# Performance work log

Measured on AMD Instinct MI355X. Metric: run time of the kernel, lower is better.

Reference implementation:

```python
import jax, jax.numpy as jnp
import numpy as np

N_QUBITS = 12
N_LAYERS = 6
BATCH = 1024


def setup_inputs() -> dict:
    key = jax.random.key(0)
    k1, k2, k3, k4 = jax.random.split(key, 4)
    x = jax.random.normal(k1, (BATCH, N_QUBITS), dtype=jnp.float32)
    weights = jax.random.normal(k2, (N_LAYERS, N_QUBITS, 3), dtype=jnp.float32)
    head_w = jax.random.normal(k3, (2, 1), dtype=jnp.float32)
    head_b = jax.random.normal(k4, (2,), dtype=jnp.float32)
    return {"x": x, "weights": weights, "head_w": head_w, "head_b": head_b}


def _apply_1q(state, U, q):
    # state: (B, 2**n) complex64; U: (2,2) or (B,2,2)
    B = state.shape[0]
    st = state.reshape(B, 1 << q, 2, -1)  # isolate qubit q
    if U.ndim == 2:
        new = jnp.einsum('ij,bajc->baic', U, st)
    else:
        new = jnp.einsum('bij,bajc->baic', U, st)
    return new.reshape(B, -1)


def _cnot_adj(state, q):
    # CNOT with control q, target q+1 (adjacent)
    B = state.shape[0]
    st = state.reshape(B, 1 << q, 2, 2, -1)
    new = jnp.concatenate([st[:, :, :1], st[:, :, 1:, ::-1]], axis=2)
    return new.reshape(B, -1)


def _rot_mat(phi, theta, omega):
    # PennyLane Rot = RZ(omega) RY(theta) RZ(phi)
    c = jnp.cos(0.5 * theta)
    s = jnp.sin(0.5 * theta)
    ep = jnp.exp(-0.5j * (phi + omega))
    em = jnp.exp(-0.5j * (phi - omega))
    row0 = jnp.stack([ep * c, -jnp.conj(em) * s])
    row1 = jnp.stack([em * s, jnp.conj(ep) * c])
    return jnp.stack([row0, row1]).astype(jnp.complex64)


def _layer(state, wl, n):
    # wl: (n, 3) Rot params for this layer, then CNOT cascade
    for q in range(n):
        state = _apply_1q(state, _rot_mat(wl[q, 0], wl[q, 1], wl[q, 2]), q)
    for q in range(n - 1):
        state = _cnot_adj(state, q)
    return state


def _circuit(x, weights):
    B, n = x.shape
    state = jnp.zeros((B, 1 << n), jnp.complex64).at[:, 0].set(1.0 + 0.0j)
    # AngleEmbedding: RX(x_q) on qubit q (batched gates)
    for q in range(n):
        h = 0.5 * x[:, q]
        c, s = jnp.cos(h), jnp.sin(h)
        U = jnp.stack([jnp.stack([c, -1j * s], -1),
                       jnp.stack([-1j * s, c], -1)], -2).astype(jnp.complex64)
        state = _apply_1q(state, U, q)
    state = jax.lax.scan(lambda s, wl: (_layer(s, wl, n), None), state, weights)[0]
    # <Z_0>
    p = jnp.abs(state.reshape(B, 2, -1)) ** 2
    return (p[:, 0].sum(-1) - p[:, 1].sum(-1)).astype(jnp.float32)


def reference(x, weights, head_w, head_b):
    z = _circuit(x, weights)            # (B,) expectation values
    q_out = z[:, None]                  # (B, 1)
    return q_out @ head_w.T + head_b    # Linear(1, 2) -> (B, 2)
```

## Files before the change

kernel.cpp:

```cpp
#include <hip/hip_runtime.h>

#define NQ 12
#define NSTATE (1 << NQ)
#define NL 6
#define TPB 512


typedef float f4 __attribute__((ext_vector_type(4)));

struct A2 { float ar, ai, br, bi; };

__device__ __forceinline__ float RL(float v, int idx) {
    return __int_as_float(__builtin_amdgcn_readlane(__float_as_int(v), idx));
}

__device__ __forceinline__ void bf2(A2& s0, A2& s1,
                                    float A, float B, float C, float D) {
    float n0r, n0i, n1r, n1i;
    n0r = fmaf(A, s0.ar, fmaf( B, s0.ai, fmaf(-C, s1.ar,  D * s1.ai)));
    n0i = fmaf(A, s0.ai, fmaf(-B, s0.ar, fmaf(-C, s1.ai, -D * s1.ar)));
    n1r = fmaf(C, s0.ar, fmaf( D, s0.ai, fmaf( A, s1.ar, -B * s1.ai)));
    n1i = fmaf(C, s0.ai, fmaf(-D, s0.ar, fmaf( A, s1.ai,  B * s1.ar)));
    s0.ar = n0r; s0.ai = n0i; s1.ar = n1r; s1.ai = n1i;
    n0r = fmaf(A, s0.br, fmaf( B, s0.bi, fmaf(-C, s1.br,  D * s1.bi)));
    n0i = fmaf(A, s0.bi, fmaf(-B, s0.br, fmaf(-C, s1.bi, -D * s1.br)));
    n1r = fmaf(C, s0.br, fmaf( D, s0.bi, fmaf( A, s1.br, -B * s1.bi)));
    n1i = fmaf(C, s0.bi, fmaf(-D, s0.br, fmaf( A, s1.bi,  B * s1.br)));
    s0.br = n0r; s0.bi = n0i; s1.br = n1r; s1.bi = n1i;
}

#define BF(i,j) bf2(a##i, a##j, A, B, C, D)
#define PK0 BF(0,1); BF(2,3); BF(4,5); BF(6,7);
#define PK1 BF(0,2); BF(1,3); BF(4,6); BF(5,7);
#define PK2 BF(0,4); BF(1,5); BF(2,6); BF(3,7);
#define GATE(qq, P) { const int gi = gb + (qq); \
    const float A = RL(gA, gi), B = RL(gB, gi), \
                C = RL(gC, gi), D = RL(gD, gi); P }

#define LDS4(off) (*(f4*)((char*)st + (off)))
#define LD1(r, ADR) { f4 v = LDS4(ADR(r)); \
    a##r.ar = v.x; a##r.ai = v.y; a##r.br = v.z; a##r.bi = v.w; }
#define ST1(r, ADR) { f4 v = {a##r.ar, a##r.ai, a##r.br, a##r.bi}; \
    LDS4(ADR(r)) = v; }
#define LD8(ADR) { LD1(0,ADR) LD1(1,ADR) LD1(2,ADR) LD1(3,ADR) \
                   LD1(4,ADR) LD1(5,ADR) LD1(6,ADR) LD1(7,ADR) }
#define ST8(ADR) { ST1(0,ADR) ST1(1,ADR) ST1(2,ADR) ST1(3,ADR) \
                   ST1(4,ADR) ST1(5,ADR) ST1(6,ADR) ST1(7,ADR) }

#define ADRA(r)  (ptAb + ((r) << 13))
#define ADRB(r)  (ptBb ^ (((r) << 10) ^ (((r) & 3) << 6)))
#define ADRC(r)  (ptCb ^ (((r) << 7) ^ (((r) >> 1) << 4)))
#define ADRD(r)  (ptDb ^ ((r) << 4))
#define GINV3(r) ((r) ^ ((r) >> 1) ^ ((r) >> 2))
#define ADRDS(r) (ptDSb ^ (GINV3(r) << 4))

#define CM(n, xr, xi, yr, yi) \
    const float n##r = fmaf(xr, yr, -(xi) * (yi)); \
    const float n##i = fmaf(xr, yi,  (xi) * (yr));
#define GCONST(q) const float A##q = RL(gA, q), B##q = RL(gB, q), \
                              C##q = RL(gC, q), D##q = RL(gD, q);
#define VQDEF(q) \
    const float v##q##0r = fmaf(A##q, c##q, -(D##q) * s##q); \
    const float v##q##0i = fmaf(-(B##q), c##q,  (C##q) * s##q); \
    const float v##q##1r = fmaf(C##q, c##q,  (B##q) * s##q); \
    const float v##q##1i = fmaf(-(D##q), c##q, -(A##q) * s##q);
#define WSEL(q, b) \
    const float w##q##r = (tj & (1 << (b))) ? v##q##1r : v##q##0r; \
    const float w##q##i = (tj & (1 << (b))) ? v##q##1i : v##q##0i;
#define SETAMP(g, rp, mm, RE, IM) \
    a##g.RE = fmaf(mm##r, Q##rp##r, -(mm##i) * Q##rp##i); \
    a##g.IM = fmaf(mm##r, Q##rp##i,  (mm##i) * Q##rp##r);

__global__ __launch_bounds__(TPB) void qsim_kernel(
    const float* __restrict__ x,
    const float* __restrict__ w,
    const float* __restrict__ hw,
    const float* __restrict__ hb,
    float* __restrict__ out)
{
    __shared__ f4 st[NSTATE];

    const int t    = threadIdx.x;
    const int lane = t & 63;
    const int e0   = blockIdx.x * 2;

    float gA, gB, gC, gD;
    {
        const float* wl = w + lane * 3;
        float phi = wl[0], th = wl[1], om = wl[2];
        float c, s, ca, sa, cb, sb;
        __sincosf(0.5f * th, &s, &c);
        __sincosf(0.5f * (phi + om), &sa, &ca);
        __sincosf(0.5f * (phi - om), &sb, &cb);
        gA = c * ca; gB = c * sa; gC = s * cb; gD = s * sb;
    }

    const int ptAb = (t ^ ((t >> 4) & 0xF)) << 4;
    const int ptBb = (((((t & 0x1C0) << 3) | (t & 0x3F)) ^ ((t >> 4) & 0x3))) << 4;
    const int ptCb = (((((t & 0x1F8) << 3) | (t & 0x7)) ^ (((t >> 3) & 0x3) << 2))) << 4;
    const int ptDb = ((t << 3) ^ ((t >> 1) & 0xF)) << 4;
    int gv = t << 3;
    gv ^= gv >> 1; gv ^= gv >> 2; gv ^= gv >> 4; gv ^= gv >> 8; gv &= 0xFFF;
    const int ptDSb = (gv ^ ((gv >> 4) & 0xF)) << 4;

    A2 a0, a1, a2, a3, a4, a5, a6, a7;

    #pragma unroll 1
    for (int k = 0; k < 4; ++k) {
        const int gb = (k + 1) * 12;

        if (k == 0) {
            const int tj = t ^ (t >> 1);
            const int t8 = (t >> 8) & 1;
            GCONST(0)  GCONST(1)  GCONST(2)  GCONST(3)
            GCONST(4)  GCONST(5)  GCONST(6)  GCONST(7)
            GCONST(8)  GCONST(9)  GCONST(10) GCONST(11)
            {
                const float* xe = x + e0 * NQ;
                float c0,s0,c1,s1,c2,s2,c3,s3,c4,s4,c5,s5;
                float c6,s6,c7,s7,c8,s8,c9,s9,c10,s10,c11,s11;
                #define EMB(q) __sincosf(0.5f * xe[q], &s##q, &c##q);
                EMB(0) EMB(1) EMB(2) EMB(3) EMB(4)  EMB(5)
                EMB(6) EMB(7) EMB(8) EMB(9) EMB(10) EMB(11)
                VQDEF(4)  WSEL(4,7)  VQDEF(5)  WSEL(5,6)
                VQDEF(6)  WSEL(6,5)  VQDEF(7)  WSEL(7,4)
                VQDEF(8)  WSEL(8,3)  VQDEF(9)  WSEL(9,2)
                VQDEF(10) WSEL(10,1) VQDEF(11) WSEL(11,0)
                CM(m45, w4r, w4i, w5r, w5i)   CM(m67, w6r, w6i, w7r, w7i)
                CM(m89, w8r, w8i, w9r, w9i)   CM(mAB, w10r, w10i, w11r, w11i)
                CM(mP, m45r, m45i, m67r, m67i) CM(mQ, m89r, m89i, mABr, mABi)
                CM(mL, mPr, mPi, mQr, mQi)
                VQDEF(3)
                const float w3ar = t8 ? v31r : v30r, w3ai = t8 ? v31i : v30i;
                const float w3br = t8 ? v30r : v31r, w3bi = t8 ? v30i : v31i;
                CM(q3a, mLr, mLi, w3ar, w3ai)  CM(q3b, mLr, mLi, w3br, w3bi)
                VQDEF(0) VQDEF(1) VQDEF(2)
                CM(H0, v00r, v00i, v10r, v10i) CM(H1, v00r, v00i, v11r, v11i)
                CM(H2, v01r, v01i, v10r, v10i) CM(H3, v01r, v01i, v11r, v11i)
                CM(Q0, H0r, H0i, v20r, v20i)   CM(Q1, H0r, H0i, v21r, v21i)
                CM(Q2, H1r, H1i, v20r, v20i)   CM(Q3, H1r, H1i, v21r, v21i)
                CM(Q4, H2r, H2i, v20r, v20i)   CM(Q5, H2r, H2i, v21r, v21i)
                CM(Q6, H3r, H3i, v20r, v20i)   CM(Q7, H3r, H3i, v21r, v21i)
                SETAMP(0,0,q3a,ar,ai) SETAMP(1,1,q3b,ar,ai)
                SETAMP(2,3,q3a,ar,ai) SETAMP(3,2,q3b,ar,ai)
                SETAMP(4,6,q3a,ar,ai) SETAMP(5,7,q3b,ar,ai)
                SETAMP(6,5,q3a,ar,ai) SETAMP(7,4,q3b,ar,ai)
            }
            {
                const float* xe = x + (e0 + 1) * NQ;
                float c0,s0,c1,s1,c2,s2,c3,s3,c4,s4,c5,s5;
                float c6,s6,c7,s7,c8,s8,c9,s9,c10,s10,c11,s11;
                EMB(0) EMB(1) EMB(2) EMB(3) EMB(4)  EMB(5)
                EMB(6) EMB(7) EMB(8) EMB(9) EMB(10) EMB(11)
                #undef EMB
                VQDEF(4)  WSEL(4,7)  VQDEF(5)  WSEL(5,6)
                VQDEF(6)  WSEL(6,5)  VQDEF(7)  WSEL(7,4)
                VQDEF(8)  WSEL(8,3)  VQDEF(9)  WSEL(9,2)
                VQDEF(10) WSEL(10,1) VQDEF(11) WSEL(11,0)
                CM(m45, w4r, w4i, w5r, w5i)   CM(m67, w6r, w6i, w7r, w7i)
                CM(m89, w8r, w8i, w9r, w9i)   CM(mAB, w10r, w10i, w11r, w11i)
                CM(mP, m45r, m45i, m67r, m67i) CM(mQ, m89r, m89i, mABr, mABi)
                CM(mL, mPr, mPi, mQr, mQi)
                VQDEF(3)
                const float w3ar = t8 ? v31r : v30r, w3ai = t8 ? v31i : v30i;
                const float w3br = t8 ? v30r : v31r, w3bi = t8 ? v30i : v31i;
                CM(q3a, mLr, mLi, w3ar, w3ai)  CM(q3b, mLr, mLi, w3br, w3bi)
                VQDEF(0) VQDEF(1) VQDEF(2)
                CM(H0, v00r, v00i, v10r, v10i) CM(H1, v00r, v00i, v11r, v11i)
                CM(H2, v01r, v01i, v10r, v10i) CM(H3, v01r, v01i, v11r, v11i)
                CM(Q0, H0r, H0i, v20r, v20i)   CM(Q1, H0r, H0i, v21r, v21i)
                CM(Q2, H1r, H1i, v20r, v20i)   CM(Q3, H1r, H1i, v21r, v21i)
                CM(Q4, H2r, H2i, v20r, v20i)   CM(Q5, H2r, H2i, v21r, v21i)
                CM(Q6, H3r, H3i, v20r, v20i)   CM(Q7, H3r, H3i, v21r, v21i)
                SETAMP(0,0,q3a,br,bi) SETAMP(1,1,q3b,br,bi)
                SETAMP(2,3,q3a,br,bi) SETAMP(3,2,q3b,br,bi)
                SETAMP(4,6,q3a,br,bi) SETAMP(5,7,q3b,br,bi)
                SETAMP(6,5,q3a,br,bi) SETAMP(7,4,q3b,br,bi)
            }
        } else {
            LD8(ADRA)
        }
        GATE(2, PK0) GATE(1, PK1) GATE(0, PK2)
        ST8(ADRA)
        __syncthreads();

        LD8(ADRB)
        GATE(5, PK0) GATE(4, PK1) GATE(3, PK2)
        ST8(ADRB)
        __syncthreads();

        LD8(ADRC)
        GATE(8, PK0) GATE(7, PK1) GATE(6, PK2)
        ST8(ADRC)
        __syncthreads();

        LD8(ADRD)
        GATE(11, PK0) GATE(10, PK1) GATE(9, PK2)
        __syncthreads();
        ST8(ADRDS)
        __syncthreads();
    }

    LD8(ADRA)
    {
        const float A = RL(gA, 60), B = RL(gB, 60),
                    C = RL(gC, 60), D = RL(gD, 60);
        bf2(a0, a4, A, B, C, D); bf2(a1, a5, A, B, C, D);
        bf2(a2, a6, A, B, C, D); bf2(a3, a7, A, B, C, D);
    }

    float za = 0.0f, zb = 0.0f;
    za += a0.ar*a0.ar + a0.ai*a0.ai;  zb += a0.br*a0.br + a0.bi*a0.bi;
    za += a1.ar*a1.ar + a1.ai*a1.ai;  zb += a1.br*a1.br + a1.bi*a1.bi;
    za += a2.ar*a2.ar + a2.ai*a2.ai;  zb += a2.br*a2.br + a2.bi*a2.bi;
    za += a3.ar*a3.ar + a3.ai*a3.ai;  zb += a3.br*a3.br + a3.bi*a3.bi;
    za -= a4.ar*a4.ar + a4.ai*a4.ai;  zb -= a4.br*a4.br + a4.bi*a4.bi;
    za -= a5.ar*a5.ar + a5.ai*a5.ai;  zb -= a5.br*a5.br + a5.bi*a5.bi;
    za -= a6.ar*a6.ar + a6.ai*a6.ai;  zb -= a6.br*a6.br + a6.bi*a6.bi;
    za -= a7.ar*a7.ar + a7.ai*a7.ai;  zb -= a7.br*a7.br + a7.bi*a7.bi;

    #pragma unroll
    for (int off = 32; off >= 1; off >>= 1) {
        za += __shfl_down(za, off);
        zb += __shfl_down(zb, off);
    }

    __syncthreads();
    float* red = (float*)st;
    if (lane == 0) { red[t >> 6] = za; red[8 + (t >> 6)] = zb; }
    __syncthreads();

    if (t == 0) {
        float zta = 0.0f, ztb = 0.0f;
        #pragma unroll
        for (int wv = 0; wv < 8; ++wv) { zta += red[wv]; ztb += red[8 + wv]; }
        out[2 * e0 + 0] = zta * hw[0] + hb[0];
        out[2 * e0 + 1] = zta * hw[1] + hb[1];
        out[2 * e0 + 2] = ztb * hw[0] + hb[0];
        out[2 * e0 + 3] = ztb * hw[1] + hb[1];
    }
}

extern "C" void kernel_launch(void* const* d_in, const int* in_sizes, int n_in,
                              void* d_out, int out_size, void* d_ws, size_t ws_size,
                              hipStream_t stream) {
    const float* x  = (const float*)d_in[0];
    const float* w  = (const float*)d_in[1];
    const float* hw = (const float*)d_in[2];
    const float* hb = (const float*)d_in[3];
    float* out = (float*)d_out;
    const int B = in_sizes[0] / NQ;
    qsim_kernel<<<B / 2, TPB, 0, stream>>>(x, w, hw, hb, out);
}
```

Baseline: 40.85 us.

## Factor Rot gates into real RY butterflies plus accumulated diagonal phases

Splits each Rot gate into its RZ parts and a real-valued RY rotation. The RZ phases from adjacent layers, carried through the CNOT cascade, are combined into one per-amplitude diagonal phase applied once per pass. Each butterfly then costs real-coefficient FMAs instead of full complex 2x2 arithmetic, which reduces VALU work in the gate passes. In exchange it adds sincos calls, many readlanes and complex products to build the phases, and it depends on subtle bookkeeping of phase indices through the CNOT permutations.

```diff
diff --git a/kernel.cpp b/kernel.cpp
--- a/kernel.cpp
+++ b/kernel.cpp
@@ -13,29 +13,29 @@
 __device__ __forceinline__ float RL(float v, int idx) {
     return __int_as_float(__builtin_amdgcn_readlane(__float_as_int(v), idx));
 }
-
-__device__ __forceinline__ void bf2(A2& s0, A2& s1,
-                                    float A, float B, float C, float D) {
-    float n0r, n0i, n1r, n1i;
-    n0r = fmaf(A, s0.ar, fmaf( B, s0.ai, fmaf(-C, s1.ar,  D * s1.ai)));
-    n0i = fmaf(A, s0.ai, fmaf(-B, s0.ar, fmaf(-C, s1.ai, -D * s1.ar)));
-    n1r = fmaf(C, s0.ar, fmaf( D, s0.ai, fmaf( A, s1.ar, -B * s1.ai)));
-    n1i = fmaf(C, s0.ai, fmaf(-D, s0.ar, fmaf( A, s1.ai,  B * s1.ar)));
-    s0.ar = n0r; s0.ai = n0i; s1.ar = n1r; s1.ai = n1i;
-    n0r = fmaf(A, s0.br, fmaf( B, s0.bi, fmaf(-C, s1.br,  D * s1.bi)));
-    n0i = fmaf(A, s0.bi, fmaf(-B, s0.br, fmaf(-C, s1.bi, -D * s1.br)));
-    n1r = fmaf(C, s0.br, fmaf( D, s0.bi, fmaf( A, s1.br, -B * s1.bi)));
-    n1i = fmaf(C, s0.bi, fmaf(-D, s0.br, fmaf( A, s1.bi,  B * s1.br)));
-    s0.br = n0r; s0.bi = n0i; s1.br = n1r; s1.bi = n1i;
-}
-
-#define BF(i,j) bf2(a##i, a##j, A, B, C, D)
+__device__ __forceinline__ float2 cmul(float2 u, float2 v) {
+    return make_float2(fmaf(u.x, v.x, -u.y * v.y),
+                       fmaf(u.x, v.y,  u.y * v.x));
+}
+
+__device__ __forceinline__ void bfy(A2& s0, A2& s1, float c, float s) {
+    float n0, n1;
+    n0 = fmaf(c, s0.ar, -s * s1.ar); n1 = fmaf(s, s0.ar, c * s1.ar);
+    s0.ar = n0; s1.ar = n1;
+    n0 = fmaf(c, s0.ai, -s * s1.ai); n1 = fmaf(s, s0.ai, c * s1.ai);
+    s0.ai = n0; s1.ai = n1;
+    n0 = fmaf(c, s0.br, -s * s1.br); n1 = fmaf(s, s0.br, c * s1.br);
+    s0.br = n0; s1.br = n1;
+    n0 = fmaf(c, s0.bi, -s * s1.bi); n1 = fmaf(s, s0.bi, c * s1.bi);
+    s0.bi = n0; s1.bi = n1;
+}
+
+#define BF(i,j) bfy(a##i, a##j, cth, sth)
 #define PK0 BF(0,1); BF(2,3); BF(4,5); BF(6,7);
 #define PK1 BF(0,2); BF(1,3); BF(4,6); BF(5,7);
 #define PK2 BF(0,4); BF(1,5); BF(2,6); BF(3,7);
-#define GATE(qq, P) { const int gi = gb + (qq); \
-    const float A = RL(gA, gi), B = RL(gB, gi), \
-                C = RL(gC, gi), D = RL(gD, gi); P }
+#define GATE(qq, P) { const float cth = RL(gc, gb + (qq)), \
+                                  sth = RL(gs, gb + (qq)); P }
 
 #define LDS4(off) (*(f4*)((char*)st + (off)))
 #define LD1(r, ADR) { f4 v = LDS4(ADR(r)); \
@@ -71,6 +71,36 @@
     a##g.RE = fmaf(mm##r, Q##rp##r, -(mm##i) * Q##rp##i); \
     a##g.IM = fmaf(mm##r, Q##rp##i,  (mm##i) * Q##rp##r);
 
+#define APW(g, Wv) { float xr = a##g.ar, xi = a##g.ai; \
+    a##g.ar = fmaf(Wv.x, xr, -Wv.y * xi); \
+    a##g.ai = fmaf(Wv.x, xi,  Wv.y * xr); \
+    xr = a##g.br; xi = a##g.bi; \
+    a##g.br = fmaf(Wv.x, xr, -Wv.y * xi); \
+    a##g.bi = fmaf(Wv.x, xi,  Wv.y * xr); }
+
+#define DTM(p) { float fv = RL(gphi, gb + 11 - (p)); \
+                 at += ((t >> (p)) & 1) ? fv : 0.0f; \
+                 float wv = RL(gom, gb - 1 - (p)); \
+                 at += ((u >> (p)) & 1) ? wv : 0.0f; }
+#define DT0(p) { float fv = RL(gphi, 23 - (p)); \
+                 a0t += ((t >> (p)) & 1) ? fv : 0.0f; }
+
+#define FBF(g,h) { \
+    float s1r = fmaf(cw, a##h.ar, -sw * a##h.ai); \
+    float s1i = fmaf(cw, a##h.ai,  sw * a##h.ar); \
+    float n0r = fmaf(c6, a##g.ar, -s6 * s1r); \
+    float n0i = fmaf(c6, a##g.ai, -s6 * s1i); \
+    a##h.ar = fmaf(s6, a##g.ar,  c6 * s1r); \
+    a##h.ai = fmaf(s6, a##g.ai,  c6 * s1i); \
+    a##g.ar = n0r; a##g.ai = n0i; \
+    s1r = fmaf(cw, a##h.br, -sw * a##h.bi); \
+    s1i = fmaf(cw, a##h.bi,  sw * a##h.br); \
+    n0r = fmaf(c6, a##g.br, -s6 * s1r); \
+    n0i = fmaf(c6, a##g.bi, -s6 * s1i); \
+    a##h.br = fmaf(s6, a##g.br,  c6 * s1r); \
+    a##h.bi = fmaf(s6, a##g.bi,  c6 * s1i); \
+    a##g.br = n0r; a##g.bi = n0i; }
+
 __global__ __launch_bounds__(TPB) void qsim_kernel(
     const float* __restrict__ x,
     const float* __restrict__ w,
@@ -85,14 +115,21 @@
     const int e0   = blockIdx.x * 2;
 
     float gA, gB, gC, gD;
+    float gc, gs;
+    float gcp, gsp, gco, gso;
+    float gphi, gom;
     {
         const float* wl = w + lane * 3;
         float phi = wl[0], th = wl[1], om = wl[2];
         float c, s, ca, sa, cb, sb;
         __sincosf(0.5f * th, &s, &c);
+        gc = c; gs = s;
         __sincosf(0.5f * (phi + om), &sa, &ca);
         __sincosf(0.5f * (phi - om), &sb, &cb);
         gA = c * ca; gB = c * sa; gC = s * cb; gD = s * sb;
+        __sincosf(phi, &gsp, &gcp);
+        __sincosf(om,  &gso, &gco);
+        gphi = phi; gom = om;
     }
 
     const int ptAb = (t ^ ((t >> 4) & 0xF)) << 4;
@@ -102,6 +139,8 @@
     int gv = t << 3;
     gv ^= gv >> 1; gv ^= gv >> 2; gv ^= gv >> 4; gv ^= gv >> 8; gv &= 0xFFF;
     const int ptDSb = (gv ^ ((gv >> 4) & 0xF)) << 4;
+
+    const int u = t ^ (t >> 1);
 
     A2 a0, a1, a2, a3, a4, a5, a6, a7;
 
@@ -177,8 +216,58 @@
                 SETAMP(4,6,q3a,br,bi) SETAMP(5,7,q3b,br,bi)
                 SETAMP(6,5,q3a,br,bi) SETAMP(7,4,q3b,br,bi)
             }
+            {
+                float a0t = 0.0f;
+                DT0(0) DT0(1) DT0(2) DT0(3) DT0(4)
+                DT0(5) DT0(6) DT0(7) DT0(8)
+                float2 P0; __sincosf(a0t, &P0.y, &P0.x);
+                const float2 Xa = make_float2(RL(gcp,14), RL(gsp,14));
+                const float2 Xb = make_float2(RL(gcp,13), RL(gsp,13));
+                const float2 Xc = make_float2(RL(gcp,12), RL(gsp,12));
+                const float2 G3 = cmul(Xa, Xb);
+                const float2 W1 = cmul(P0, Xa), W2 = cmul(P0, Xb);
+                const float2 W3 = cmul(P0, G3), W4 = cmul(P0, Xc);
+                const float2 W5 = cmul(W4, Xa), W6 = cmul(W4, Xb);
+                const float2 W7 = cmul(W4, G3);
+                APW(0, P0) APW(1, W1) APW(2, W2) APW(3, W3)
+                APW(4, W4) APW(5, W5) APW(6, W6) APW(7, W7)
+            }
         } else {
             LD8(ADRA)
+            {
+                float at = 0.0f;
+                DTM(0) DTM(1) DTM(2) DTM(3)
+                DTM(4) DTM(5) DTM(6) DTM(7)
+                { float f8 = RL(gphi, gb + 3); at += (t & 256) ? f8 : 0.0f; }
+                const float w8 = RL(gom, gb - 9);
+                const float ae = at + ((t & 256) ? w8 : 0.0f);
+                const float ao = at + ((t & 256) ? 0.0f : w8);
+                float2 Pe, Po;
+                __sincosf(ae, &Pe.y, &Pe.x);
+                __sincosf(ao, &Po.y, &Po.x);
+                const float2 Xp9  = make_float2(RL(gcp, gb+2),  RL(gsp, gb+2));
+                const float2 Xw9  = make_float2(RL(gco, gb-10), RL(gso, gb-10));
+                const float2 Xp10 = make_float2(RL(gcp, gb+1),  RL(gsp, gb+1));
+                const float2 Xw10 = make_float2(RL(gco, gb-11), RL(gso, gb-11));
+                const float2 Xp11 = make_float2(RL(gcp, gb+0),  RL(gsp, gb+0));
+                const float2 Xw11 = make_float2(RL(gco, gb-12), RL(gso, gb-12));
+                const float2 Y11 = cmul(Xp11, Xw11);
+                const float2 F1 = cmul(Xp9, Xw9);
+                const float2 Bf = cmul(Xw9, Xp10);
+                const float2 F2 = cmul(Bf, Xw10);
+                const float2 Cf = cmul(Xp9, Xp10);
+                const float2 F3 = cmul(Cf, Xw10);
+                const float2 F4 = cmul(Xw10, Y11);
+                const float2 F5 = cmul(F1, F4);
+                const float2 F6 = cmul(Bf, Y11);
+                const float2 F7 = cmul(Cf, Y11);
+                const float2 W1 = cmul(Po, F1), W2 = cmul(Pe, F2);
+                const float2 W3 = cmul(Po, F3), W4 = cmul(Pe, F4);
+                const float2 W5 = cmul(Po, F5), W6 = cmul(Pe, F6);
+                const float2 W7 = cmul(Po, F7);
+                APW(0, Pe) APW(1, W1) APW(2, W2) APW(3, W3)
+                APW(4, W4) APW(5, W5) APW(6, W6) APW(7, W7)
+            }
         }
         GATE(2, PK0) GATE(1, PK1) GATE(0, PK2)
         ST8(ADRA)
@@ -203,10 +292,10 @@
 
     LD8(ADRA)
     {
-        const float A = RL(gA, 60), B = RL(gB, 60),
-                    C = RL(gC, 60), D = RL(gD, 60);
-        bf2(a0, a4, A, B, C, D); bf2(a1, a5, A, B, C, D);
-        bf2(a2, a6, A, B, C, D); bf2(a3, a7, A, B, C, D);
+        const float th0 = RL(gom, 48) + RL(gphi, 60);
+        float cw, sw; __sincosf(th0, &sw, &cw);
+        const float c6 = RL(gc, 60), s6 = RL(gs, 60);
+        FBF(0,4) FBF(1,5) FBF(2,6) FBF(3,7)
     }
 
     float za = 0.0f, zb = 0.0f;
```

Measured after the change: 40.68 us. Within noise of the previous version (-0.4%).

## Process 16 amplitudes per thread with 4-qubit passes and 256 threads

Applied to the files above, without the earlier changes.

Each thread now holds 16 amplitude pairs instead of 8, so each LDS round trip applies four qubit gates instead of three. That cuts the passes per layer-group from four to three and the barriers accordingly, with 256 threads per block. The swizzled address maps and the initial product-state construction are reworked to match. This doubles per-thread register use (16 A2 structs), which may lower occupancy, and halves the threads available per block.

```diff
diff --git a/kernel.cpp b/kernel.cpp
--- a/kernel.cpp
+++ b/kernel.cpp
@@ -2,8 +2,7 @@
 
 #define NQ 12
 #define NSTATE (1 << NQ)
-#define NL 6
-#define TPB 512
+#define TPB 256
 
 
 typedef float f4 __attribute__((ext_vector_type(4)));
@@ -30,9 +29,14 @@
 }
 
 #define BF(i,j) bf2(a##i, a##j, A, B, C, D)
-#define PK0 BF(0,1); BF(2,3); BF(4,5); BF(6,7);
-#define PK1 BF(0,2); BF(1,3); BF(4,6); BF(5,7);
-#define PK2 BF(0,4); BF(1,5); BF(2,6); BF(3,7);
+#define PK0 BF(0,1); BF(2,3); BF(4,5); BF(6,7); \
+            BF(8,9); BF(10,11); BF(12,13); BF(14,15);
+#define PK1 BF(0,2); BF(1,3); BF(4,6); BF(5,7); \
+            BF(8,10); BF(9,11); BF(12,14); BF(13,15);
+#define PK2 BF(0,4); BF(1,5); BF(2,6); BF(3,7); \
+            BF(8,12); BF(9,13); BF(10,14); BF(11,15);
+#define PK3 BF(0,8); BF(1,9); BF(2,10); BF(3,11); \
+            BF(4,12); BF(5,13); BF(6,14); BF(7,15);
 #define GATE(qq, P) { const int gi = gb + (qq); \
     const float A = RL(gA, gi), B = RL(gB, gi), \
                 C = RL(gC, gi), D = RL(gD, gi); P }
@@ -42,17 +46,20 @@
     a##r.ar = v.x; a##r.ai = v.y; a##r.br = v.z; a##r.bi = v.w; }
 #define ST1(r, ADR) { f4 v = {a##r.ar, a##r.ai, a##r.br, a##r.bi}; \
     LDS4(ADR(r)) = v; }
-#define LD8(ADR) { LD1(0,ADR) LD1(1,ADR) LD1(2,ADR) LD1(3,ADR) \
-                   LD1(4,ADR) LD1(5,ADR) LD1(6,ADR) LD1(7,ADR) }
-#define ST8(ADR) { ST1(0,ADR) ST1(1,ADR) ST1(2,ADR) ST1(3,ADR) \
-                   ST1(4,ADR) ST1(5,ADR) ST1(6,ADR) ST1(7,ADR) }
-
-#define ADRA(r)  (ptAb + ((r) << 13))
-#define ADRB(r)  (ptBb ^ (((r) << 10) ^ (((r) & 3) << 6)))
-#define ADRC(r)  (ptCb ^ (((r) << 7) ^ (((r) >> 1) << 4)))
-#define ADRD(r)  (ptDb ^ ((r) << 4))
-#define GINV3(r) ((r) ^ ((r) >> 1) ^ ((r) >> 2))
-#define ADRDS(r) (ptDSb ^ (GINV3(r) << 4))
+#define LD16(ADR) { LD1(0,ADR) LD1(1,ADR) LD1(2,ADR) LD1(3,ADR) \
+                    LD1(4,ADR) LD1(5,ADR) LD1(6,ADR) LD1(7,ADR) \
+                    LD1(8,ADR) LD1(9,ADR) LD1(10,ADR) LD1(11,ADR) \
+                    LD1(12,ADR) LD1(13,ADR) LD1(14,ADR) LD1(15,ADR) }
+#define ST16(ADR) { ST1(0,ADR) ST1(1,ADR) ST1(2,ADR) ST1(3,ADR) \
+                    ST1(4,ADR) ST1(5,ADR) ST1(6,ADR) ST1(7,ADR) \
+                    ST1(8,ADR) ST1(9,ADR) ST1(10,ADR) ST1(11,ADR) \
+                    ST1(12,ADR) ST1(13,ADR) ST1(14,ADR) ST1(15,ADR) }
+
+#define ADRA(r)   (ptAb + ((r) << 12))
+#define ADRB(r)   (ptBb ^ (((r) << 8) ^ ((r) << 4)))
+#define ADRC(r)   (ptCb ^ ((r) << 4))
+#define GINV4(r)  ((r) ^ ((r) >> 1) ^ ((r) >> 2) ^ ((r) >> 3))
+#define ADRCS(r)  (ptCSb ^ (GINV4(r) << 4))
 
 #define CM(n, xr, xi, yr, yi) \
     const float n##r = fmaf(xr, yr, -(xi) * (yi)); \
@@ -95,15 +102,15 @@
         gA = c * ca; gB = c * sa; gC = s * cb; gD = s * sb;
     }
 
-    const int ptAb = (t ^ ((t >> 4) & 0xF)) << 4;
-    const int ptBb = (((((t & 0x1C0) << 3) | (t & 0x3F)) ^ ((t >> 4) & 0x3))) << 4;
-    const int ptCb = (((((t & 0x1F8) << 3) | (t & 0x7)) ^ (((t >> 3) & 0x3) << 2))) << 4;
-    const int ptDb = ((t << 3) ^ ((t >> 1) & 0xF)) << 4;
-    int gv = t << 3;
+    const int ptAb  = (t ^ (t >> 4)) << 4;
+    const int ptBb  = ((((t & 0xF0) << 4) | (t & 0x0F))) << 4;
+    const int ptCb  = (((t << 4) ^ (t & 0x0F))) << 4;
+    int gv = t << 4;
     gv ^= gv >> 1; gv ^= gv >> 2; gv ^= gv >> 4; gv ^= gv >> 8; gv &= 0xFFF;
-    const int ptDSb = (gv ^ ((gv >> 4) & 0xF)) << 4;
-
-    A2 a0, a1, a2, a3, a4, a5, a6, a7;
+    const int ptCSb = (gv ^ ((gv >> 4) & 0xF)) << 4;
+
+    A2 a0, a1, a2, a3, a4, a5, a6, a7,
+       a8, a9, a10, a11, a12, a13, a14, a15;
 
     #pragma unroll 1
     for (int k = 0; k < 4; ++k) {
@@ -111,7 +118,7 @@
 
         if (k == 0) {
             const int tj = t ^ (t >> 1);
-            const int t8 = (t >> 8) & 1;
+            const int t7 = (t >> 7) & 1;
             GCONST(0)  GCONST(1)  GCONST(2)  GCONST(3)
             GCONST(4)  GCONST(5)  GCONST(6)  GCONST(7)
             GCONST(8)  GCONST(9)  GCONST(10) GCONST(11)
@@ -122,18 +129,21 @@
                 #define EMB(q) __sincosf(0.5f * xe[q], &s##q, &c##q);
                 EMB(0) EMB(1) EMB(2) EMB(3) EMB(4)  EMB(5)
                 EMB(6) EMB(7) EMB(8) EMB(9) EMB(10) EMB(11)
-                VQDEF(4)  WSEL(4,7)  VQDEF(5)  WSEL(5,6)
-                VQDEF(6)  WSEL(6,5)  VQDEF(7)  WSEL(7,4)
-                VQDEF(8)  WSEL(8,3)  VQDEF(9)  WSEL(9,2)
-                VQDEF(10) WSEL(10,1) VQDEF(11) WSEL(11,0)
-                CM(m45, w4r, w4i, w5r, w5i)   CM(m67, w6r, w6i, w7r, w7i)
-                CM(m89, w8r, w8i, w9r, w9i)   CM(mAB, w10r, w10i, w11r, w11i)
-                CM(mP, m45r, m45i, m67r, m67i) CM(mQ, m89r, m89i, mABr, mABi)
+                VQDEF(5)  WSEL(5,6)  VQDEF(6)  WSEL(6,5)
+                VQDEF(7)  WSEL(7,4)  VQDEF(8)  WSEL(8,3)
+                VQDEF(9)  WSEL(9,2)  VQDEF(10) WSEL(10,1)
+                VQDEF(11) WSEL(11,0)
+                CM(m56, w5r, w5i, w6r, w6i)   CM(m78, w7r, w7i, w8r, w8i)
+                CM(m9A, w9r, w9i, w10r, w10i)
+                CM(mP, m56r, m56i, m78r, m78i) CM(mQ, m9Ar, m9Ai, w11r, w11i)
                 CM(mL, mPr, mPi, mQr, mQi)
+                VQDEF(4)
+                const float w4ar = t7 ? v41r : v40r, w4ai = t7 ? v41i : v40i;
+                const float w4br = t7 ? v40r : v41r, w4bi = t7 ? v40i : v41i;
+                CM(Pa, mLr, mLi, w4ar, w4ai)   CM(Pb, mLr, mLi, w4br, w4bi)
                 VQDEF(3)
-                const float w3ar = t8 ? v31r : v30r, w3ai = t8 ? v31i : v30i;
-                const float w3br = t8 ? v30r : v31r, w3bi = t8 ? v30i : v31i;
-                CM(q3a, mLr, mLi, w3ar, w3ai)  CM(q3b, mLr, mLi, w3br, w3bi)
+                CM(T00, Par, Pai, v30r, v30i)  CM(T01, Par, Pai, v31r, v31i)
+                CM(T10, Pbr, Pbi, v31r, v31i)  CM(T11, Pbr, Pbi, v30r, v30i)
                 VQDEF(0) VQDEF(1) VQDEF(2)
                 CM(H0, v00r, v00i, v10r, v10i) CM(H1, v00r, v00i, v11r, v11i)
                 CM(H2, v01r, v01i, v10r, v10i) CM(H3, v01r, v01i, v11r, v11i)
@@ -141,10 +151,14 @@
                 CM(Q2, H1r, H1i, v20r, v20i)   CM(Q3, H1r, H1i, v21r, v21i)
                 CM(Q4, H2r, H2i, v20r, v20i)   CM(Q5, H2r, H2i, v21r, v21i)
                 CM(Q6, H3r, H3i, v20r, v20i)   CM(Q7, H3r, H3i, v21r, v21i)
-                SETAMP(0,0,q3a,ar,ai) SETAMP(1,1,q3b,ar,ai)
-                SETAMP(2,3,q3a,ar,ai) SETAMP(3,2,q3b,ar,ai)
-                SETAMP(4,6,q3a,ar,ai) SETAMP(5,7,q3b,ar,ai)
-                SETAMP(6,5,q3a,ar,ai) SETAMP(7,4,q3b,ar,ai)
+                SETAMP(0,0,T00,ar,ai)  SETAMP(1,0,T10,ar,ai)
+                SETAMP(2,1,T01,ar,ai)  SETAMP(3,1,T11,ar,ai)
+                SETAMP(4,3,T00,ar,ai)  SETAMP(5,3,T10,ar,ai)
+                SETAMP(6,2,T01,ar,ai)  SETAMP(7,2,T11,ar,ai)
+                SETAMP(8,6,T00,ar,ai)  SETAMP(9,6,T10,ar,ai)
+                SETAMP(10,7,T01,ar,ai) SETAMP(11,7,T11,ar,ai)
+                SETAMP(12,5,T00,ar,ai) SETAMP(13,5,T10,ar,ai)
+                SETAMP(14,4,T01,ar,ai) SETAMP(15,4,T11,ar,ai)
             }
             {
                 const float* xe = x + (e0 + 1) * NQ;
@@ -153,18 +167,21 @@
                 EMB(0) EMB(1) EMB(2) EMB(3) EMB(4)  EMB(5)
                 EMB(6) EMB(7) EMB(8) EMB(9) EMB(10) EMB(11)
                 #undef EMB
-                VQDEF(4)  WSEL(4,7)  VQDEF(5)  WSEL(5,6)
-                VQDEF(6)  WSEL(6,5)  VQDEF(7)  WSEL(7,4)
-                VQDEF(8)  WSEL(8,3)  VQDEF(9)  WSEL(9,2)
-                VQDEF(10) WSEL(10,1) VQDEF(11) WSEL(11,0)
-                CM(m45, w4r, w4i, w5r, w5i)   CM(m67, w6r, w6i, w7r, w7i)
-                CM(m89, w8r, w8i, w9r, w9i)   CM(mAB, w10r, w10i, w11r, w11i)
-                CM(mP, m45r, m45i, m67r, m67i) CM(mQ, m89r, m89i, mABr, mABi)
+                VQDEF(5)  WSEL(5,6)  VQDEF(6)  WSEL(6,5)
+                VQDEF(7)  WSEL(7,4)  VQDEF(8)  WSEL(8,3)
+                VQDEF(9)  WSEL(9,2)  VQDEF(10) WSEL(10,1)
+                VQDEF(11) WSEL(11,0)
+                CM(m56, w5r, w5i, w6r, w6i)   CM(m78, w7r, w7i, w8r, w8i)
+                CM(m9A, w9r, w9i, w10r, w10i)
+                CM(mP, m56r, m56i, m78r, m78i) CM(mQ, m9Ar, m9Ai, w11r, w11i)
                 CM(mL, mPr, mPi, mQr, mQi)
+                VQDEF(4)
+                const float w4ar = t7 ? v41r : v40r, w4ai = t7 ? v41i : v40i;
+                const float w4br = t7 ? v40r : v41r, w4bi = t7 ? v40i : v41i;
+                CM(Pa, mLr, mLi, w4ar, w4ai)   CM(Pb, mLr, mLi, w4br, w4bi)
                 VQDEF(3)
-                const float w3ar = t8 ? v31r : v30r, w3ai = t8 ? v31i : v30i;
-                const float w3br = t8 ? v30r : v31r, w3bi = t8 ? v30i : v31i;
-                CM(q3a, mLr, mLi, w3ar, w3ai)  CM(q3b, mLr, mLi, w3br, w3bi)
+                CM(T00, Par, Pai, v30r, v30i)  CM(T01, Par, Pai, v31r, v31i)
+                CM(T10, Pbr, Pbi, v31r, v31i)  CM(T11, Pbr, Pbi, v30r, v30i)
                 VQDEF(0) VQDEF(1) VQDEF(2)
                 CM(H0, v00r, v00i, v10r, v10i) CM(H1, v00r, v00i, v11r, v11i)
                 CM(H2, v01r, v01i, v10r, v10i) CM(H3, v01r, v01i, v11r, v11i)
@@ -172,52 +189,61 @@
                 CM(Q2, H1r, H1i, v20r, v20i)   CM(Q3, H1r, H1i, v21r, v21i)
                 CM(Q4, H2r, H2i, v20r, v20i)   CM(Q5, H2r, H2i, v21r, v21i)
                 CM(Q6, H3r, H3i, v20r, v20i)   CM(Q7, H3r, H3i, v21r, v21i)
-                SETAMP(0,0,q3a,br,bi) SETAMP(1,1,q3b,br,bi)
-                SETAMP(2,3,q3a,br,bi) SETAMP(3,2,q3b,br,bi)
-                SETAMP(4,6,q3a,br,bi) SETAMP(5,7,q3b,br,bi)
-                SETAMP(6,5,q3a,br,bi) SETAMP(7,4,q3b,br,bi)
+                SETAMP(0,0,T00,br,bi)  SETAMP(1,0,T10,br,bi)
+                SETAMP(2,1,T01,br,bi)  SETAMP(3,1,T11,br,bi)
+                SETAMP(4,3,T00,br,bi)  SETAMP(5,3,T10,br,bi)
+                SETAMP(6,2,T01,br,bi)  SETAMP(7,2,T11,br,bi)
+                SETAMP(8,6,T00,br,bi)  SETAMP(9,6,T10,br,bi)
+                SETAMP(10,7,T01,br,bi) SETAMP(11,7,T11,br,bi)
+                SETAMP(12,5,T00,br,bi) SETAMP(13,5,T10,br,bi)
+                SETAMP(14,4,T01,br,bi) SETAMP(15,4,T11,br,bi)
             }
         } else {
-            LD8(ADRA)
+            LD16(ADRA)
         }
-        GATE(2, PK0) GATE(1, PK1) GATE(0, PK2)
-        ST8(ADRA)
-        __syncthreads();
-
-        LD8(ADRB)
-        GATE(5, PK0) GATE(4, PK1) GATE(3, PK2)
-        ST8(ADRB)
-        __syncthreads();
-
-        LD8(ADRC)
-        GATE(8, PK0) GATE(7, PK1) GATE(6, PK2)
-        ST8(ADRC)
-        __syncthreads();
-
-        LD8(ADRD)
-        GATE(11, PK0) GATE(10, PK1) GATE(9, PK2)
-        __syncthreads();
-        ST8(ADRDS)
-        __syncthreads();
-    }
-
-    LD8(ADRA)
+        GATE(3, PK0) GATE(2, PK1) GATE(1, PK2) GATE(0, PK3)
+        ST16(ADRA)
+        __syncthreads();
+
+        LD16(ADRB)
+        GATE(7, PK0) GATE(6, PK1) GATE(5, PK2) GATE(4, PK3)
+        ST16(ADRB)
+        __syncthreads();
+
+        LD16(ADRC)
+        GATE(11, PK0) GATE(10, PK1) GATE(9, PK2) GATE(8, PK3)
+        __syncthreads();
+        ST16(ADRCS)
+        __syncthreads();
+    }
+
+    LD16(ADRA)
     {
         const float A = RL(gA, 60), B = RL(gB, 60),
                     C = RL(gC, 60), D = RL(gD, 60);
-        bf2(a0, a4, A, B, C, D); bf2(a1, a5, A, B, C, D);
-        bf2(a2, a6, A, B, C, D); bf2(a3, a7, A, B, C, D);
+        bf2(a0, a8,  A, B, C, D); bf2(a1, a9,  A, B, C, D);
+        bf2(a2, a10, A, B, C, D); bf2(a3, a11, A, B, C, D);
+        bf2(a4, a12, A, B, C, D); bf2(a5, a13, A, B, C, D);
+        bf2(a6, a14, A, B, C, D); bf2(a7, a15, A, B, C, D);
     }
 
     float za = 0.0f, zb = 0.0f;
-    za += a0.ar*a0.ar + a0.ai*a0.ai;  zb += a0.br*a0.br + a0.bi*a0.bi;
-    za += a1.ar*a1.ar + a1.ai*a1.ai;  zb += a1.br*a1.br + a1.bi*a1.bi;
-    za += a2.ar*a2.ar + a2.ai*a2.ai;  zb += a2.br*a2.br + a2.bi*a2.bi;
-    za += a3.ar*a3.ar + a3.ai*a3.ai;  zb += a3.br*a3.br + a3.bi*a3.bi;
-    za -= a4.ar*a4.ar + a4.ai*a4.ai;  zb -= a4.br*a4.br + a4.bi*a4.bi;
-    za -= a5.ar*a5.ar + a5.ai*a5.ai;  zb -= a5.br*a5.br + a5.bi*a5.bi;
-    za -= a6.ar*a6.ar + a6.ai*a6.ai;  zb -= a6.br*a6.br + a6.bi*a6.bi;
-    za -= a7.ar*a7.ar + a7.ai*a7.ai;  zb -= a7.br*a7.br + a7.bi*a7.bi;
+    za += a0.ar*a0.ar + a0.ai*a0.ai;    zb += a0.br*a0.br + a0.bi*a0.bi;
+    za += a1.ar*a1.ar + a1.ai*a1.ai;    zb += a1.br*a1.br + a1.bi*a1.bi;
+    za += a2.ar*a2.ar + a2.ai*a2.ai;    zb += a2.br*a2.br + a2.bi*a2.bi;
+    za += a3.ar*a3.ar + a3.ai*a3.ai;    zb += a3.br*a3.br + a3.bi*a3.bi;
+    za += a4.ar*a4.ar + a4.ai*a4.ai;    zb += a4.br*a4.br + a4.bi*a4.bi;
+    za += a5.ar*a5.ar + a5.ai*a5.ai;    zb += a5.br*a5.br + a5.bi*a5.bi;
+    za += a6.ar*a6.ar + a6.ai*a6.ai;    zb += a6.br*a6.br + a6.bi*a6.bi;
+    za += a7.ar*a7.ar + a7.ai*a7.ai;    zb += a7.br*a7.br + a7.bi*a7.bi;
+    za -= a8.ar*a8.ar + a8.ai*a8.ai;    zb -= a8.br*a8.br + a8.bi*a8.bi;
+    za -= a9.ar*a9.ar + a9.ai*a9.ai;    zb -= a9.br*a9.br + a9.bi*a9.bi;
+    za -= a10.ar*a10.ar + a10.ai*a10.ai; zb -= a10.br*a10.br + a10.bi*a10.bi;
+    za -= a11.ar*a11.ar + a11.ai*a11.ai; zb -= a11.br*a11.br + a11.bi*a11.bi;
+    za -= a12.ar*a12.ar + a12.ai*a12.ai; zb -= a12.br*a12.br + a12.bi*a12.bi;
+    za -= a13.ar*a13.ar + a13.ai*a13.ai; zb -= a13.br*a13.br + a13.bi*a13.bi;
+    za -= a14.ar*a14.ar + a14.ai*a14.ai; zb -= a14.br*a14.br + a14.bi*a14.bi;
+    za -= a15.ar*a15.ar + a15.ai*a15.ai; zb -= a15.br*a15.br + a15.bi*a15.bi;
 
     #pragma unroll
     for (int off = 32; off >= 1; off >>= 1) {
@@ -227,13 +253,12 @@
 
     __syncthreads();
     float* red = (float*)st;
-    if (lane == 0) { red[t >> 6] = za; red[8 + (t >> 6)] = zb; }
+    if (lane == 0) { red[t >> 6] = za; red[4 + (t >> 6)] = zb; }
     __syncthreads();
 
     if (t == 0) {
-        float zta = 0.0f, ztb = 0.0f;
-        #pragma unroll
-        for (int wv = 0; wv < 8; ++wv) { zta += red[wv]; ztb += red[8 + wv]; }
+        float zta = red[0] + red[1] + red[2] + red[3];
+        float ztb = red[4] + red[5] + red[6] + red[7];
         out[2 * e0 + 0] = zta * hw[0] + hb[0];
         out[2 * e0 + 1] = zta * hw[1] + hb[1];
         out[2 * e0 + 2] = ztb * hw[0] + hb[0];
```

Result: faster. 39.56 us (-3.1%).
